# Performance work log

Hardware: AMD Instinct MI355X
Metric: run time of the kernel (lower is better)

## Reference

```python
import jax, jax.numpy as jnp
import numpy as np
from jax import lax

B, T, F, U = 1, 8000, 512, 512


def _lstm(x, h0, c0, W, R, b):
    """Keras-default LSTM: gates ordered (i,f,g,o), sigmoid recurrent act, tanh act.
    x: [B,T,F], h0/c0: [B,U], W: [F,4U], R: [U,4U], b: [4U].
    Returns (seq_out [B,T,U], h [B,U], c [B,U])."""
    xz = jnp.einsum('btf,fg->btg', x, W) + b  # precompute input projections [B,T,4U]

    def step(carry, xz_t):
        h, c = carry
        z = xz_t + h @ R
        i, f, g, o = jnp.split(z, 4, axis=-1)
        c = jax.nn.sigmoid(f) * c + jax.nn.sigmoid(i) * jnp.tanh(g)
        h = jax.nn.sigmoid(o) * jnp.tanh(c)
        return (h, c), h

    (h, c), hs = lax.scan(step, (h0, c0), jnp.swapaxes(xz, 0, 1))  # scan over time
    return jnp.swapaxes(hs, 0, 1), h, c


def setup_inputs() -> dict:
    key = jax.random.key(0)
    ks = jax.random.split(key, 9)
    s_w = 1.0 / np.sqrt(F)
    s_r = 1.0 / np.sqrt(U)
    return {
        'in_real': jax.random.normal(ks[0], (B, T, F), jnp.float32),
        'in_imag': jax.random.normal(ks[1], (B, T, F), jnp.float32),
        'in_states': jax.random.normal(ks[2], (B, 4, U, 2), jnp.float32),
        'Wr': jax.random.normal(ks[3], (F, 4 * U), jnp.float32) * s_w,
        'Rr': jax.random.normal(ks[4], (U, 4 * U), jnp.float32) * s_r,
        'br': jnp.zeros((4 * U,), jnp.float32),
        'Wi': jax.random.normal(ks[5], (F, 4 * U), jnp.float32) * s_w,
        'Ri': jax.random.normal(ks[6], (U, 4 * U), jnp.float32) * s_r,
        'bi': jnp.zeros((4 * U,), jnp.float32),
    }


def reference(in_real, in_imag, in_states, Wr, Rr, br, Wi, Ri, bi):
    # four coupled passes sharing the two (real/imag) LSTM weight sets
    r2r, h0, c0 = _lstm(in_real, in_states[:, 0, :, 0], in_states[:, 0, :, 1], Wr, Rr, br)
    r2i, h1, c1 = _lstm(in_real, in_states[:, 1, :, 0], in_states[:, 1, :, 1], Wi, Ri, bi)
    i2r, h2, c2 = _lstm(in_imag, in_states[:, 2, :, 0], in_states[:, 2, :, 1], Wr, Rr, br)
    i2i, h3, c3 = _lstm(in_imag, in_states[:, 3, :, 0], in_states[:, 3, :, 1], Wi, Ri, bi)
    out_h = jnp.stack([h0, h1, h2, h3], axis=0).reshape(1, 4, U)
    out_c = jnp.stack([c0, c1, c2, c3], axis=0).reshape(1, 4, U)
    out_states = jnp.stack([out_h, out_c], axis=-1)  # [1,4,U,2]
    real_out = r2r - i2i
    imag_out = i2r + r2i
    return real_out, imag_out, out_states
```

## Files before the change

### kernel.cpp

```cpp
#include <hip/hip_runtime.h>

#define T_TOTAL 8000

typedef unsigned long long ull;

__device__ __forceinline__ float sig_f(float x) { return 1.f / (1.f + __expf(-x)); }
__device__ __forceinline__ float tanh_f(float x) { return 1.f - 2.f / (__expf(2.f * x) + 1.f); }

__global__ void init_kernel(const float* __restrict__ st, ull* hp, float* cs) {
  int idx = blockIdx.x * blockDim.x + threadIdx.x;
  if (idx < 2048) {
    unsigned hb = __float_as_uint(st[2 * idx + 0]);
    hp[idx]        = ((ull)hb << 32) | 0ull;
    hp[2048 + idx] = 0ull;
    cs[idx] = st[2 * idx + 1];
  }
}

__global__ __launch_bounds__(256) void proj_kernel(
    const float* __restrict__ in_real, const float* __restrict__ in_imag,
    const float* __restrict__ Wr, const float* __restrict__ br,
    const float* __restrict__ Wi, const float* __restrict__ bi,
    float* __restrict__ xz, int t0, int chunk) {
  const int p = blockIdx.z;
  const float* __restrict__ X = (p < 2) ? in_real : in_imag;
  const float* __restrict__ W = (p & 1) ? Wi : Wr;
  const float* __restrict__ Bv = (p & 1) ? bi : br;
  const int nb = blockIdx.x * 64, mb = blockIdx.y * 64;
  __shared__ float As[16][68];
  __shared__ float Bs[16][68];
  const int tid = threadIdx.x;
  const int tm = tid >> 4, tn = tid & 15;
  const int lam = tid >> 2, lak = (tid & 3) << 2;
  const int lbk = tid >> 4, lbn = (tid & 15) << 2;
  float acc[4][4] = {};
  for (int k0 = 0; k0 < 512; k0 += 16) {
    int msafe = mb + lam; if (msafe > chunk - 1) msafe = chunk - 1;
    float4 a4 = *(const float4*)&X[(size_t)(t0 + msafe) * 512 + k0 + lak];
    float4 b4 = *(const float4*)&W[(size_t)(k0 + lbk) * 2048 + nb + lbn];
    __syncthreads();
    As[lak + 0][lam] = a4.x; As[lak + 1][lam] = a4.y;
    As[lak + 2][lam] = a4.z; As[lak + 3][lam] = a4.w;
    *(float4*)&Bs[lbk][lbn] = b4;
    __syncthreads();
#pragma unroll
    for (int k = 0; k < 16; ++k) {
      float4 av = *(const float4*)&As[k][tm << 2];
      float4 bv = *(const float4*)&Bs[k][tn << 2];
      acc[0][0] = fmaf(av.x, bv.x, acc[0][0]); acc[0][1] = fmaf(av.x, bv.y, acc[0][1]);
      acc[0][2] = fmaf(av.x, bv.z, acc[0][2]); acc[0][3] = fmaf(av.x, bv.w, acc[0][3]);
      acc[1][0] = fmaf(av.y, bv.x, acc[1][0]); acc[1][1] = fmaf(av.y, bv.y, acc[1][1]);
      acc[1][2] = fmaf(av.y, bv.z, acc[1][2]); acc[1][3] = fmaf(av.y, bv.w, acc[1][3]);
      acc[2][0] = fmaf(av.z, bv.x, acc[2][0]); acc[2][1] = fmaf(av.z, bv.y, acc[2][1]);
      acc[2][2] = fmaf(av.z, bv.z, acc[2][2]); acc[2][3] = fmaf(av.z, bv.w, acc[2][3]);
      acc[3][0] = fmaf(av.w, bv.x, acc[3][0]); acc[3][1] = fmaf(av.w, bv.y, acc[3][1]);
      acc[3][2] = fmaf(av.w, bv.z, acc[3][2]); acc[3][3] = fmaf(av.w, bv.w, acc[3][3]);
    }
  }
  float4 bias4 = *(const float4*)&Bv[nb + (tn << 2)];
#pragma unroll
  for (int i = 0; i < 4; ++i) {
    int mm = mb + (tm << 2) + i;
    if (mm < chunk) {
      float4 v;
      v.x = acc[i][0] + bias4.x; v.y = acc[i][1] + bias4.y;
      v.z = acc[i][2] + bias4.z; v.w = acc[i][3] + bias4.w;
      *(float4*)&xz[(size_t)(p * chunk + mm) * 2048 + nb + (tn << 2)] = v;
    }
  }
}

__global__ __launch_bounds__(256, 1) void recur_kernel(
    const float* __restrict__ xz, const float* __restrict__ Rr, const float* __restrict__ Ri,
    ull* hp, float* cs, float* __restrict__ hseq, int t0, int chunk) {
  const int tid = threadIdx.x;
  const int w = tid >> 6, l = tid & 63;
  const int un = l & 3, kg = l >> 2;
  const int p = blockIdx.x & 3, g = blockIdx.x >> 2;
  const int U0w = g * 16 + w * 4;
  const float* __restrict__ R = (p & 1) ? Ri : Rr;

  float r[4][32];
  {
    const float* Rb = R + (size_t)(kg * 32) * 2048 + (U0w + un);
#pragma unroll
    for (int kk = 0; kk < 32; ++kk) {
#pragma unroll
      for (int gg = 0; gg < 4; ++gg) r[gg][kk] = Rb[(size_t)kk * 2048 + gg * 512];
    }
  }

  __shared__ float hsh[2][16 * 36];
  const int wrow = w * 4 + (l >> 4);
  const int wcol = (2 * l) & 31;
  float c_old = cs[p * 512 + U0w + un];

  float xzn[4];
  {
    const float* xr = xz + (size_t)p * chunk * 2048 + (U0w + un);
#pragma unroll
    for (int gg = 0; gg < 4; ++gg) xzn[gg] = xr[gg * 512];
  }

  for (int tl = 0; tl < chunk; ++tl) {
    const int t = t0 + tl;
    float xzv[4];
#pragma unroll
    for (int gg = 0; gg < 4; ++gg) xzv[gg] = xzn[gg];

    const ull* gp = hp + (t & 1) * 2048 + p * 512 + w * 128 + 2 * l;
    const unsigned tgt = (unsigned)t;
    ull q0, q1;
    for (;;) {
      q0 = __hip_atomic_load(gp + 0, __ATOMIC_RELAXED, __HIP_MEMORY_SCOPE_AGENT);
      q1 = __hip_atomic_load(gp + 1, __ATOMIC_RELAXED, __HIP_MEMORY_SCOPE_AGENT);
      if (__all(((unsigned)q0 == tgt) & ((unsigned)q1 == tgt))) break;
    }

    {
      float2 hv2 = make_float2(__uint_as_float((unsigned)(q0 >> 32)),
                               __uint_as_float((unsigned)(q1 >> 32)));
      *(float2*)&hsh[t & 1][wrow * 36 + wcol] = hv2;
    }
    asm volatile("s_waitcnt lgkmcnt(0)" ::: "memory");
    __builtin_amdgcn_s_barrier();
    asm volatile("" ::: "memory");

    if (tl + 1 < chunk) {
      const float* xr = xz + ((size_t)p * chunk + tl + 1) * 2048 + (U0w + un);
#pragma unroll
      for (int gg = 0; gg < 4; ++gg) xzn[gg] = xr[gg * 512];
    }

    const float* rp = &hsh[t & 1][kg * 36];
    float a[4] = {0.f, 0.f, 0.f, 0.f};
#pragma unroll
    for (int q = 0; q < 8; ++q) {
      float4 h4 = *(const float4*)(rp + 4 * q);
#pragma unroll
      for (int gg = 0; gg < 4; ++gg) {
        a[gg] = fmaf(r[gg][4 * q + 0], h4.x, a[gg]);
        a[gg] = fmaf(r[gg][4 * q + 1], h4.y, a[gg]);
        a[gg] = fmaf(r[gg][4 * q + 2], h4.z, a[gg]);
        a[gg] = fmaf(r[gg][4 * q + 3], h4.w, a[gg]);
      }
    }
#pragma unroll
    for (int gg = 0; gg < 4; ++gg) {
      a[gg] += __shfl_xor(a[gg], 4);
      a[gg] += __shfl_xor(a[gg], 8);
      a[gg] += __shfl_xor(a[gg], 16);
      a[gg] += __shfl_xor(a[gg], 32);
    }
    const float zi = a[0] + xzv[0], zf = a[1] + xzv[1];
    const float zg = a[2] + xzv[2], zo = a[3] + xzv[3];
    const float cn = sig_f(zf) * c_old + sig_f(zi) * tanh_f(zg);
    const float hn = sig_f(zo) * tanh_f(cn);
    c_old = cn;

    if (l < 4) {
      ull pv = ((ull)__float_as_uint(hn) << 32) | (ull)(unsigned)(t + 1);
      __hip_atomic_store(&hp[((t + 1) & 1) * 2048 + p * 512 + U0w + l], pv,
                         __ATOMIC_RELAXED, __HIP_MEMORY_SCOPE_AGENT);
      hseq[((size_t)p * chunk + tl) * 512 + U0w + l] = hn;
    }
  }
  if (l < 4) cs[p * 512 + U0w + l] = c_old;
}

__global__ __launch_bounds__(256) void combine_kernel(
    const float* __restrict__ hseq, float* __restrict__ out, int t0, int chunk) {
  const size_t n4 = (size_t)chunk * 512 / 4;
  const size_t idx = (size_t)blockIdx.x * 256 + threadIdx.x;
  if (idx >= n4) return;
  const size_t pstride = (size_t)chunk * 512;
  float4 h0 = *(const float4*)&hseq[0 * pstride + 4 * idx];
  float4 h1 = *(const float4*)&hseq[1 * pstride + 4 * idx];
  float4 h2 = *(const float4*)&hseq[2 * pstride + 4 * idx];
  float4 h3 = *(const float4*)&hseq[3 * pstride + 4 * idx];
  float4 re, im;
  re.x = h0.x - h3.x; re.y = h0.y - h3.y; re.z = h0.z - h3.z; re.w = h0.w - h3.w;
  im.x = h1.x + h2.x; im.y = h1.y + h2.y; im.z = h1.z + h2.z; im.w = h1.w + h2.w;
  *(float4*)&out[(size_t)t0 * 512 + 4 * idx] = re;
  *(float4*)&out[(size_t)4096000 + (size_t)t0 * 512 + 4 * idx] = im;
}

__global__ void final_kernel(const float* __restrict__ hseq, const float* __restrict__ cs,
                             float* __restrict__ out, int chunk) {
  int idx = blockIdx.x * blockDim.x + threadIdx.x;
  if (idx < 2048) {
    const int p = idx >> 9, u = idx & 511;
    out[8192000 + 2 * (size_t)idx + 0] = hseq[((size_t)p * chunk + (chunk - 1)) * 512 + u];
    out[8192000 + 2 * (size_t)idx + 1] = cs[idx];
  }
}

extern "C" void kernel_launch(void* const* d_in, const int* in_sizes, int n_in,
                              void* d_out, int out_size, void* d_ws, size_t ws_size,
                              hipStream_t stream) {
  (void)in_sizes; (void)n_in;
  const float* in_real   = (const float*)d_in[0];
  const float* in_imag   = (const float*)d_in[1];
  const float* in_states = (const float*)d_in[2];
  const float* Wr = (const float*)d_in[3];
  const float* Rr = (const float*)d_in[4];
  const float* br = (const float*)d_in[5];
  const float* Wi = (const float*)d_in[6];
  const float* Ri = (const float*)d_in[7];
  const float* bi = (const float*)d_in[8];
  float* out = (float*)d_out;

  ull* hp = (ull*)d_ws;
  float* cs = (float*)((char*)d_ws + 32768);
  float* xz = (float*)((char*)d_ws + 65536);

  int chunk = 2000;
  while (chunk > 125 && (size_t)chunk * 40960 + 65536 > ws_size) chunk >>= 1;
  float* hseq = xz + (size_t)4 * chunk * 2048;

  hipMemsetAsync(d_out, 0, (size_t)out_size * sizeof(float), stream);
  init_kernel<<<2, 1024, 0, stream>>>(in_states, hp, cs);
  for (int t0 = 0; t0 < T_TOTAL; t0 += chunk) {
    dim3 pgrid(2048 / 64, (chunk + 63) / 64, 4);
    proj_kernel<<<pgrid, 256, 0, stream>>>(in_real, in_imag, Wr, br, Wi, bi, xz, t0, chunk);
    recur_kernel<<<128, 256, 0, stream>>>(xz, Rr, Ri, hp, cs, hseq, t0, chunk);
    combine_kernel<<<(chunk * 512 / 4 + 255) / 256, 256, 0, stream>>>(hseq, out, t0, chunk);
  }
  final_kernel<<<2, 1024, 0, stream>>>(hseq, cs, out, chunk);
}
```

Before: 12.93 ms.

## Use single-wave recurrence blocks and drop the per-step workgroup barrier

The recurrent kernel now launches 512 one-wave blocks instead of 128 four-wave blocks. Each wave polls and loads all 512 hidden values it needs with wide dwordx4 system-coherent loads, then stages them in a single LDS buffer. This removes the per-timestep s_barrier between waves. The cost is four times more global polling traffic per step and 512 persistent blocks that must all be co-resident. Without the barrier, correctness within the wave depends on the lockstep wave execution and the lgkmcnt wait before the shared-memory reads.

```diff
diff --git a/kernel.cpp b/kernel.cpp
--- a/kernel.cpp
+++ b/kernel.cpp
@@ -70,14 +70,14 @@
   }
 }
 
-__global__ __launch_bounds__(256, 1) void recur_kernel(
+__global__ __launch_bounds__(64, 1) void recur_kernel(
     const float* __restrict__ xz, const float* __restrict__ Rr, const float* __restrict__ Ri,
     ull* hp, float* cs, float* __restrict__ hseq, int t0, int chunk) {
-  const int tid = threadIdx.x;
-  const int w = tid >> 6, l = tid & 63;
+  const int l = threadIdx.x & 63;
   const int un = l & 3, kg = l >> 2;
-  const int p = blockIdx.x & 3, g = blockIdx.x >> 2;
-  const int U0w = g * 16 + w * 4;
+  const int bx = blockIdx.x;
+  const int p = bx & 3;
+  const int U0w = (bx >> 2) * 4;
   const float* __restrict__ R = (p & 1) ? Ri : Rr;
 
   float r[4][32];
@@ -90,9 +90,8 @@
     }
   }
 
-  __shared__ float hsh[2][16 * 36];
-  const int wrow = w * 4 + (l >> 4);
-  const int wcol = (2 * l) & 31;
+  __shared__ float hsh[16 * 36];
+  const int srow = l >> 2, scol = (8 * l) & 31;
   float c_old = cs[p * 512 + U0w + un];
 
   float xzn[4];
@@ -108,23 +107,37 @@
 #pragma unroll
     for (int gg = 0; gg < 4; ++gg) xzv[gg] = xzn[gg];
 
-    const ull* gp = hp + (t & 1) * 2048 + p * 512 + w * 128 + 2 * l;
+    const ull* gp = hp + (t & 1) * 2048 + p * 512 + 8 * l;
     const unsigned tgt = (unsigned)t;
-    ull q0, q1;
+    ulonglong2 A, B, C, D;
     for (;;) {
-      q0 = __hip_atomic_load(gp + 0, __ATOMIC_RELAXED, __HIP_MEMORY_SCOPE_AGENT);
-      q1 = __hip_atomic_load(gp + 1, __ATOMIC_RELAXED, __HIP_MEMORY_SCOPE_AGENT);
-      if (__all(((unsigned)q0 == tgt) & ((unsigned)q1 == tgt))) break;
+      asm volatile(
+          "global_load_dwordx4 %0, %4, off sc0 sc1\n\t"
+          "global_load_dwordx4 %1, %4, off offset:16 sc0 sc1\n\t"
+          "global_load_dwordx4 %2, %4, off offset:32 sc0 sc1\n\t"
+          "global_load_dwordx4 %3, %4, off offset:48 sc0 sc1\n\t"
+          "s_waitcnt vmcnt(0)"
+          : "=&v"(A), "=&v"(B), "=&v"(C), "=&v"(D) : "v"(gp) : "memory");
+      unsigned ok = (unsigned)((unsigned)A.x == tgt) & (unsigned)((unsigned)A.y == tgt) &
+                    (unsigned)((unsigned)B.x == tgt) & (unsigned)((unsigned)B.y == tgt) &
+                    (unsigned)((unsigned)C.x == tgt) & (unsigned)((unsigned)C.y == tgt) &
+                    (unsigned)((unsigned)D.x == tgt) & (unsigned)((unsigned)D.y == tgt);
+      if (__all(ok)) break;
     }
 
     {
-      float2 hv2 = make_float2(__uint_as_float((unsigned)(q0 >> 32)),
-                               __uint_as_float((unsigned)(q1 >> 32)));
-      *(float2*)&hsh[t & 1][wrow * 36 + wcol] = hv2;
+      float4 h0 = make_float4(__uint_as_float((unsigned)(A.x >> 32)),
+                              __uint_as_float((unsigned)(A.y >> 32)),
+                              __uint_as_float((unsigned)(B.x >> 32)),
+                              __uint_as_float((unsigned)(B.y >> 32)));
+      float4 h1 = make_float4(__uint_as_float((unsigned)(C.x >> 32)),
+                              __uint_as_float((unsigned)(C.y >> 32)),
+                              __uint_as_float((unsigned)(D.x >> 32)),
+                              __uint_as_float((unsigned)(D.y >> 32)));
+      *(float4*)&hsh[srow * 36 + scol] = h0;
+      *(float4*)&hsh[srow * 36 + scol + 4] = h1;
     }
     asm volatile("s_waitcnt lgkmcnt(0)" ::: "memory");
-    __builtin_amdgcn_s_barrier();
-    asm volatile("" ::: "memory");
 
     if (tl + 1 < chunk) {
       const float* xr = xz + ((size_t)p * chunk + tl + 1) * 2048 + (U0w + un);
@@ -132,7 +145,7 @@
       for (int gg = 0; gg < 4; ++gg) xzn[gg] = xr[gg * 512];
     }
 
-    const float* rp = &hsh[t & 1][kg * 36];
+    const float* rp = &hsh[kg * 36];
     float a[4] = {0.f, 0.f, 0.f, 0.f};
 #pragma unroll
     for (int q = 0; q < 8; ++q) {
@@ -223,7 +236,7 @@
   for (int t0 = 0; t0 < T_TOTAL; t0 += chunk) {
     dim3 pgrid(2048 / 64, (chunk + 63) / 64, 4);
     proj_kernel<<<pgrid, 256, 0, stream>>>(in_real, in_imag, Wr, br, Wi, bi, xz, t0, chunk);
-    recur_kernel<<<128, 256, 0, stream>>>(xz, Rr, Ri, hp, cs, hseq, t0, chunk);
+    recur_kernel<<<512, 64, 0, stream>>>(xz, Rr, Ri, hp, cs, hseq, t0, chunk);
     combine_kernel<<<(chunk * 512 / 4 + 255) / 256, 256, 0, stream>>>(hseq, out, t0, chunk);
   }
   final_kernel<<<2, 1024, 0, stream>>>(hseq, cs, out, chunk);
```

New measurement: 15.14 ms. 17.1% more time.
